# Kernel optimization log

Hardware: AMD Instinct MI355X
Metric: run time of the kernel (lower is better)

## Reference

```python
import jax, jax.numpy as jnp
import numpy as np

B, S, H, I, E, TOP_K = 2, 1024, 1024, 2048, 8, 2


def setup_inputs() -> dict:
    key = jax.random.key(0)
    ks = jax.random.split(key, 5)
    return {
        "hidden_states": jax.random.normal(ks[0], (B, S, H), jnp.float32),
        # torch Linear weights are (out, in)
        "router_w": jax.random.normal(ks[1], (E, H), jnp.float32) * 0.02,
        "w1": jax.random.normal(ks[2], (E, I, H), jnp.float32) * 0.02,
        "v": jax.random.normal(ks[3], (E, I, H), jnp.float32) * 0.02,
        "w2": jax.random.normal(ks[4], (E, H, I), jnp.float32) * 0.02,
    }


def _moe(x, router_w, w1, v, w2):
    # x: [T, H] flattened tokens
    T = x.shape[0]
    n_exp = router_w.shape[0]
    logits = x @ router_w.T                                    # [T, E]
    probs = jax.nn.softmax(logits.astype(jnp.float32), axis=-1)
    top_p, top_i = jax.lax.top_k(probs, TOP_K)                 # [T, K]
    top_p = top_p / top_p.sum(axis=-1, keepdims=True)
    top_p = top_p.astype(x.dtype)
    # dense gate matrix [T, E]; zero for unselected experts -> identical math
    # to the torch gather / index_add combine
    gates = jnp.zeros((T, n_exp), x.dtype).at[
        jnp.arange(T)[:, None], top_i].set(top_p)
    out = jnp.zeros_like(x)
    for e in range(n_exp):  # small fixed expert loop keeps peak memory low
        h = jax.nn.gelu(x @ w1[e].T, approximate=False) * (x @ v[e].T)  # [T, I]
        out = out + gates[:, e:e + 1] * (h @ w2[e].T)                   # [T, H]
    return out, logits


def reference(hidden_states, router_w, w1, v, w2):
    b, s, h = hidden_states.shape
    out, logits = _moe(hidden_states.reshape(-1, h), router_w, w1, v, w2)
    return out.reshape(b, s, h), logits
```

## Files before the change

### kernel.cpp

```cpp
#include <hip/hip_runtime.h>
#include <math.h>

#define T 2048
#define HD 1024
#define ID 2048
#define NE 8
#define CSTRIDE 32

typedef short bf16x8 __attribute__((ext_vector_type(8)));
typedef float f32x4 __attribute__((ext_vector_type(4)));
typedef unsigned short u16x4 __attribute__((ext_vector_type(4)));

__device__ __forceinline__ unsigned short f2bf(float f) {
  union { float f; unsigned u; } v; v.f = f;
  unsigned r = v.u + 0x7FFFu + ((v.u >> 16) & 1u);
  return (unsigned short)(r >> 16);
}

__device__ __forceinline__ void cast_chunk16(const float* __restrict__ s,
                                             unsigned short* __restrict__ d,
                                             size_t base) {
  size_t o = base + (size_t)threadIdx.x * 4;
#pragma unroll
  for (int k = 0; k < 4; k++) {
    float4 f = *(const float4*)(s + o + k * 1024);
    u16x4 h;
    h[0] = f2bf(f.x); h[1] = f2bf(f.y); h[2] = f2bf(f.z); h[3] = f2bf(f.w);
    *(u16x4*)(d + o + k * 1024) = h;
  }
}

__device__ __forceinline__ void glds16(const unsigned short* g, unsigned short* l) {
  __builtin_amdgcn_global_load_lds(
      (const __attribute__((address_space(1))) unsigned int*)(g),
      (__attribute__((address_space(3))) unsigned int*)(l), 16, 0, 0);
}

__global__ __launch_bounds__(256) void prep_kernel(
    const float* __restrict__ x, const float* __restrict__ rw,
    const float* __restrict__ w1, const float* __restrict__ v,
    unsigned short* __restrict__ xb, unsigned short* __restrict__ w1b,
    unsigned short* __restrict__ vb, float* __restrict__ logits_out,
    int* __restrict__ pair_rowid, float* __restrict__ pair_gate,
    int* __restrict__ counts) {
  int bx = blockIdx.x;
  if (bx >= 768) {
    int cid = bx - 768;
    const float* s = (cid < 4096) ? w1 : v;
    unsigned short* d = (cid < 4096) ? w1b : vb;
    cast_chunk16(s, d, (size_t)(cid & 4095) * 4096);
    return;
  }
  if (bx >= 256) {
    cast_chunk16(x, xb, (size_t)(bx - 256) * 4096);
    return;
  }
  __shared__ int s_e[16];
  __shared__ int s_rid[16];
  __shared__ float s_gt[16];
  int tid = threadIdx.x;
  int wid = tid >> 6, lane = tid & 63;
  for (int tk = 0; tk < 2; ++tk) {
    int t = bx * 8 + wid * 2 + tk;
    float acc[NE];
#pragma unroll
    for (int e = 0; e < NE; e++) acc[e] = 0.f;
    const float* xrow = x + (size_t)t * HD;
#pragma unroll 2
    for (int j = 0; j < HD; j += 64) {
      float xv = xrow[j + lane];
#pragma unroll
      for (int e = 0; e < NE; e++) acc[e] += xv * rw[e * HD + j + lane];
    }
#pragma unroll
    for (int e = 0; e < NE; e++)
      for (int off = 32; off > 0; off >>= 1) acc[e] += __shfl_xor(acc[e], off, 64);
    if (lane == 0) {
#pragma unroll
      for (int e = 0; e < NE; e++) logits_out[t * NE + e] = acc[e];
      int e0 = 0;
#pragma unroll
      for (int e = 1; e < NE; e++) if (acc[e] > acc[e0]) e0 = e;
      int e1 = (e0 == 0) ? 1 : 0;
#pragma unroll
      for (int e = 0; e < NE; e++)
        if (e != e0 && e != e1 && acc[e] > acc[e1]) e1 = e;
      float b = __expf(acc[e1] - acc[e0]);
      float g0 = 1.f / (1.f + b);
      float g1 = 1.f - g0;
      int slot = (wid * 2 + tk) * 2;
      s_e[slot] = e0; s_rid[slot] = t * 2;     s_gt[slot] = g0;
      s_e[slot + 1] = e1; s_rid[slot + 1] = t * 2 + 1; s_gt[slot + 1] = g1;
    }
  }
  __syncthreads();
  if (tid < NE) {
    int cnt = 0;
#pragma unroll
    for (int k = 0; k < 16; k++) if (s_e[k] == tid) cnt++;
    if (cnt) {
      int base = atomicAdd(&counts[tid * CSTRIDE], cnt);
      int p = 0;
      for (int k = 0; k < 16; k++)
        if (s_e[k] == tid) {
          pair_rowid[tid * T + base + p] = s_rid[k];
          pair_gate[tid * T + base + p] = s_gt[k];
          p++;
        }
    }
  }
}

__global__ __launch_bounds__(256) void gemm1_kernel(
    const unsigned short* __restrict__ xb, const unsigned short* __restrict__ w1b,
    const unsigned short* __restrict__ vb, unsigned short* __restrict__ hb,
    const float* __restrict__ w2, unsigned short* __restrict__ w2b,
    const int* __restrict__ pair_rowid, const int* __restrict__ counts) {
  if (blockIdx.x >= 32) {
    int cid = (blockIdx.x - 32) + 32 * (blockIdx.y + 16 * blockIdx.z);
    cast_chunk16(w2, w2b, (size_t)cid * 4096);
    return;
  }
  int e = blockIdx.z;
  int cnt = counts[e * CSTRIDE];
  int row0 = blockIdx.y * 128;
  if (row0 >= cnt) return;
  __shared__ unsigned short As[128 * 64];
  __shared__ unsigned short B1s[64 * 64];
  __shared__ unsigned short B2s[64 * 64];
  __shared__ int rids[128];
  int tid = threadIdx.x;
  if (tid < 128) {
    int idx = row0 + tid; if (idx > cnt - 1) idx = cnt - 1;
    rids[tid] = pair_rowid[e * T + idx];
  }
  __syncthreads();
  int lane = tid & 63, wid = tid >> 6;
  int wr = wid >> 1, wc = wid & 1;
  int col0 = blockIdx.x * 64;
  int gr = lane >> 3, gc = lane & 7;
  const unsigned short *aA[4], *aB1[2], *aB2[2];
#pragma unroll
  for (int c = 0; c < 4; c++) {
    int row = (c * 4 + wid) * 8 + gr;
    int tok = rids[row] >> 1;
    aA[c] = xb + (size_t)tok * HD + ((gc ^ (row & 7)) * 8);
  }
#pragma unroll
  for (int c = 0; c < 2; c++) {
    int row = (c * 4 + wid) * 8 + gr;
    int kswz = ((gc ^ (row & 7)) * 8);
    aB1[c] = w1b + ((size_t)(e * ID + col0 + row)) * HD + kswz;
    aB2[c] = vb  + ((size_t)(e * ID + col0 + row)) * HD + kswz;
  }
  f32x4 acc1[4][2] = {};
  f32x4 acc3[4][2] = {};
  int mrow = lane & 15, kq = lane >> 4;
  int swzm = mrow & 7;
  for (int kt = 0; kt < HD; kt += 64) {
#pragma unroll
    for (int c = 0; c < 4; c++)
      glds16(aA[c] + kt, &As[(c * 4 + wid) * 512]);
#pragma unroll
    for (int c = 0; c < 2; c++) {
      glds16(aB1[c] + kt, &B1s[(c * 4 + wid) * 512]);
      glds16(aB2[c] + kt, &B2s[(c * 4 + wid) * 512]);
    }
    __syncthreads();
#pragma unroll
    for (int kk = 0; kk < 2; kk++) {
      int g = kk * 4 + kq;
      int ko = ((g ^ swzm) * 8);
      bf16x8 a[4], b1[2], b2[2];
#pragma unroll
      for (int mi = 0; mi < 4; mi++)
        a[mi] = *(const bf16x8*)&As[(wr * 64 + mi * 16 + mrow) * 64 + ko];
#pragma unroll
      for (int ni = 0; ni < 2; ni++) {
        b1[ni] = *(const bf16x8*)&B1s[(wc * 32 + ni * 16 + mrow) * 64 + ko];
        b2[ni] = *(const bf16x8*)&B2s[(wc * 32 + ni * 16 + mrow) * 64 + ko];
      }
#pragma unroll
      for (int mi = 0; mi < 4; mi++)
#pragma unroll
        for (int ni = 0; ni < 2; ni++) {
          acc1[mi][ni] = __builtin_amdgcn_mfma_f32_16x16x32_bf16(a[mi], b1[ni], acc1[mi][ni], 0, 0, 0);
          acc3[mi][ni] = __builtin_amdgcn_mfma_f32_16x16x32_bf16(a[mi], b2[ni], acc3[mi][ni], 0, 0, 0);
        }
    }
    __syncthreads();
  }
  int dcol = lane & 15, drow4 = (lane >> 4) * 4;
#pragma unroll
  for (int mi = 0; mi < 4; mi++)
#pragma unroll
    for (int ni = 0; ni < 2; ni++)
#pragma unroll
      for (int r = 0; r < 4; r++) {
        int lr = wr * 64 + mi * 16 + drow4 + r;
        if (row0 + lr < cnt) {
          float g1v = acc1[mi][ni][r];
          float g3v = acc3[mi][ni][r];
          float hval = 0.5f * g1v * (1.f + erff(g1v * 0.70710678118654752f)) * g3v;
          int rowid = rids[lr];
          hb[(size_t)rowid * ID + col0 + wc * 32 + ni * 16 + dcol] = f2bf(hval);
        }
      }
}

__global__ __launch_bounds__(256) void gemm2_kernel(
    const unsigned short* __restrict__ hb, const unsigned short* __restrict__ w2b,
    float* __restrict__ yb, const int* __restrict__ pair_rowid,
    const float* __restrict__ pair_gate, const int* __restrict__ counts) {
  int e = blockIdx.z;
  int cnt = counts[e * CSTRIDE];
  int row0 = blockIdx.y * 128;
  if (row0 >= cnt) return;
  __shared__ unsigned short As[128 * 64];
  __shared__ unsigned short Bs[64 * 64];
  __shared__ int rids[128];
  __shared__ float gts[128];
  int tid = threadIdx.x;
  if (tid < 128) {
    int idx = row0 + tid; if (idx > cnt - 1) idx = cnt - 1;
    rids[tid] = pair_rowid[e * T + idx];
    gts[tid] = pair_gate[e * T + idx];
  }
  __syncthreads();
  int lane = tid & 63, wid = tid >> 6;
  int wr = wid >> 1, wc = wid & 1;
  int col0 = blockIdx.x * 64;
  int gr = lane >> 3, gc = lane & 7;
  const unsigned short *aA[4], *aB[2];
#pragma unroll
  for (int c = 0; c < 4; c++) {
    int row = (c * 4 + wid) * 8 + gr;
    aA[c] = hb + (size_t)rids[row] * ID + ((gc ^ (row & 7)) * 8);
  }
#pragma unroll
  for (int c = 0; c < 2; c++) {
    int row = (c * 4 + wid) * 8 + gr;
    int kswz = ((gc ^ (row & 7)) * 8);
    aB[c] = w2b + ((size_t)(e * HD + col0 + row)) * ID + kswz;
  }
  f32x4 acc[4][2] = {};
  int mrow = lane & 15, kq = lane >> 4;
  int swzm = mrow & 7;
  for (int kt = 0; kt < ID; kt += 64) {
#pragma unroll
    for (int c = 0; c < 4; c++)
      glds16(aA[c] + kt, &As[(c * 4 + wid) * 512]);
#pragma unroll
    for (int c = 0; c < 2; c++)
      glds16(aB[c] + kt, &Bs[(c * 4 + wid) * 512]);
    __syncthreads();
#pragma unroll
    for (int kk = 0; kk < 2; kk++) {
      int g = kk * 4 + kq;
      int ko = ((g ^ swzm) * 8);
      bf16x8 a[4], b[2];
#pragma unroll
      for (int mi = 0; mi < 4; mi++)
        a[mi] = *(const bf16x8*)&As[(wr * 64 + mi * 16 + mrow) * 64 + ko];
#pragma unroll
      for (int ni = 0; ni < 2; ni++)
        b[ni] = *(const bf16x8*)&Bs[(wc * 32 + ni * 16 + mrow) * 64 + ko];
#pragma unroll
      for (int mi = 0; mi < 4; mi++)
#pragma unroll
        for (int ni = 0; ni < 2; ni++)
          acc[mi][ni] = __builtin_amdgcn_mfma_f32_16x16x32_bf16(a[mi], b[ni], acc[mi][ni], 0, 0, 0);
    }
    __syncthreads();
  }
  int dcol = lane & 15, drow4 = (lane >> 4) * 4;
#pragma unroll
  for (int mi = 0; mi < 4; mi++)
#pragma unroll
    for (int ni = 0; ni < 2; ni++)
#pragma unroll
      for (int r = 0; r < 4; r++) {
        int lr = wr * 64 + mi * 16 + drow4 + r;
        if (row0 + lr < cnt) {
          float val = gts[lr] * acc[mi][ni][r];
          yb[(size_t)rids[lr] * HD + col0 + wc * 32 + ni * 16 + dcol] = val;
        }
      }
}

__global__ __launch_bounds__(256) void combine_kernel(
    const float* __restrict__ yb, float* __restrict__ out) {
  size_t t = blockIdx.x;
  int c = threadIdx.x * 4;
  float4 a = *(const float4*)(yb + (t * 2) * HD + c);
  float4 b = *(const float4*)(yb + (t * 2 + 1) * HD + c);
  float4 o;
  o.x = a.x + b.x; o.y = a.y + b.y; o.z = a.z + b.z; o.w = a.w + b.w;
  *(float4*)(out + t * HD + c) = o;
}

extern "C" void kernel_launch(void* const* d_in, const int* in_sizes, int n_in,
                              void* d_out, int out_size, void* d_ws, size_t ws_size,
                              hipStream_t stream) {
  const float* x  = (const float*)d_in[0];
  const float* rw = (const float*)d_in[1];
  const float* w1 = (const float*)d_in[2];
  const float* v  = (const float*)d_in[3];
  const float* w2 = (const float*)d_in[4];
  float* out = (float*)d_out;
  float* logits_out = out + (size_t)T * HD;

  char* ws = (char*)d_ws;
  unsigned short* xb  = (unsigned short*)(ws);
  unsigned short* hb  = (unsigned short*)(ws + (4u << 20));
  unsigned short* w1b = (unsigned short*)(ws + (20u << 20));
  unsigned short* vb  = (unsigned short*)(ws + (52u << 20));
  unsigned short* w2b = (unsigned short*)(ws + (84u << 20));
  float* yb           = (float*)(ws + (20u << 20));
  int*   pair_rowid   = (int*)  (ws + (116u << 20));
  float* pair_gate    = (float*)(ws + (116u << 20) + 65536);
  int*   counts       = (int*)  (ws + (116u << 20) + 131072);

  hipMemsetAsync(counts, 0, NE * CSTRIDE * sizeof(int), stream);

  prep_kernel<<<8960, 256, 0, stream>>>(x, rw, w1, v, xb, w1b, vb,
                                        logits_out, pair_rowid, pair_gate,
                                        counts);
  gemm1_kernel<<<dim3(ID / 64 + 32, T / 128, NE), 256, 0, stream>>>(
      xb, w1b, vb, hb, w2, w2b, pair_rowid, counts);
  gemm2_kernel<<<dim3(HD / 64, T / 128, NE), 256, 0, stream>>>(
      hb, w2b, yb, pair_rowid, pair_gate, counts);
  combine_kernel<<<T, 256, 0, stream>>>(yb, out);
}
```

Measured before the change: 320.5 us.

## Split gemm2 over K halves and widen the N tile to 128 columns

The down-projection kernel now computes a 128x128 output tile per block, reusing each loaded A tile across two B tiles, and splits the K=2048 reduction into two halves on separate blocks. Each half writes its partial result to its own yb buffer, and the combine kernel sums four partials instead of two. The aim is to cut redundant reads of the gathered hidden rows and keep enough blocks in flight. The cost is twice the yb write traffic, extra combine reads, and more accumulator registers per thread.

```diff
diff --git a/kernel.cpp b/kernel.cpp
--- a/kernel.cpp
+++ b/kernel.cpp
@@ -212,12 +212,13 @@
     const unsigned short* __restrict__ hb, const unsigned short* __restrict__ w2b,
     float* __restrict__ yb, const int* __restrict__ pair_rowid,
     const float* __restrict__ pair_gate, const int* __restrict__ counts) {
-  int e = blockIdx.z;
+  int e = blockIdx.z >> 1, kh = blockIdx.z & 1;
   int cnt = counts[e * CSTRIDE];
   int row0 = blockIdx.y * 128;
   if (row0 >= cnt) return;
   __shared__ unsigned short As[128 * 64];
-  __shared__ unsigned short Bs[64 * 64];
+  __shared__ unsigned short B1s[64 * 64];
+  __shared__ unsigned short B2s[64 * 64];
   __shared__ int rids[128];
   __shared__ float gts[128];
   int tid = threadIdx.x;
@@ -229,51 +230,60 @@
   __syncthreads();
   int lane = tid & 63, wid = tid >> 6;
   int wr = wid >> 1, wc = wid & 1;
-  int col0 = blockIdx.x * 64;
+  int col0 = blockIdx.x * 128;
   int gr = lane >> 3, gc = lane & 7;
-  const unsigned short *aA[4], *aB[2];
+  const unsigned short *aA[4], *aB1[2], *aB2[2];
 #pragma unroll
   for (int c = 0; c < 4; c++) {
     int row = (c * 4 + wid) * 8 + gr;
-    aA[c] = hb + (size_t)rids[row] * ID + ((gc ^ (row & 7)) * 8);
+    aA[c] = hb + (size_t)rids[row] * ID + kh * 1024 + ((gc ^ (row & 7)) * 8);
   }
 #pragma unroll
   for (int c = 0; c < 2; c++) {
     int row = (c * 4 + wid) * 8 + gr;
     int kswz = ((gc ^ (row & 7)) * 8);
-    aB[c] = w2b + ((size_t)(e * HD + col0 + row)) * ID + kswz;
-  }
-  f32x4 acc[4][2] = {};
+    aB1[c] = w2b + ((size_t)(e * HD + col0 + row)) * ID + kh * 1024 + kswz;
+    aB2[c] = w2b + ((size_t)(e * HD + col0 + 64 + row)) * ID + kh * 1024 + kswz;
+  }
+  f32x4 acc1[4][2] = {};
+  f32x4 acc3[4][2] = {};
   int mrow = lane & 15, kq = lane >> 4;
   int swzm = mrow & 7;
-  for (int kt = 0; kt < ID; kt += 64) {
+  for (int kt = 0; kt < 1024; kt += 64) {
 #pragma unroll
     for (int c = 0; c < 4; c++)
       glds16(aA[c] + kt, &As[(c * 4 + wid) * 512]);
 #pragma unroll
-    for (int c = 0; c < 2; c++)
-      glds16(aB[c] + kt, &Bs[(c * 4 + wid) * 512]);
+    for (int c = 0; c < 2; c++) {
+      glds16(aB1[c] + kt, &B1s[(c * 4 + wid) * 512]);
+      glds16(aB2[c] + kt, &B2s[(c * 4 + wid) * 512]);
+    }
     __syncthreads();
 #pragma unroll
     for (int kk = 0; kk < 2; kk++) {
       int g = kk * 4 + kq;
       int ko = ((g ^ swzm) * 8);
-      bf16x8 a[4], b[2];
+      bf16x8 a[4], b1[2], b2[2];
 #pragma unroll
       for (int mi = 0; mi < 4; mi++)
         a[mi] = *(const bf16x8*)&As[(wr * 64 + mi * 16 + mrow) * 64 + ko];
 #pragma unroll
-      for (int ni = 0; ni < 2; ni++)
-        b[ni] = *(const bf16x8*)&Bs[(wc * 32 + ni * 16 + mrow) * 64 + ko];
+      for (int ni = 0; ni < 2; ni++) {
+        b1[ni] = *(const bf16x8*)&B1s[(wc * 32 + ni * 16 + mrow) * 64 + ko];
+        b2[ni] = *(const bf16x8*)&B2s[(wc * 32 + ni * 16 + mrow) * 64 + ko];
+      }
 #pragma unroll
       for (int mi = 0; mi < 4; mi++)
 #pragma unroll
-        for (int ni = 0; ni < 2; ni++)
-          acc[mi][ni] = __builtin_amdgcn_mfma_f32_16x16x32_bf16(a[mi], b[ni], acc[mi][ni], 0, 0, 0);
+        for (int ni = 0; ni < 2; ni++) {
+          acc1[mi][ni] = __builtin_amdgcn_mfma_f32_16x16x32_bf16(a[mi], b1[ni], acc1[mi][ni], 0, 0, 0);
+          acc3[mi][ni] = __builtin_amdgcn_mfma_f32_16x16x32_bf16(a[mi], b2[ni], acc3[mi][ni], 0, 0, 0);
+        }
     }
     __syncthreads();
   }
   int dcol = lane & 15, drow4 = (lane >> 4) * 4;
+  float* ybh = yb + (size_t)kh * (2 * T) * HD;
 #pragma unroll
   for (int mi = 0; mi < 4; mi++)
 #pragma unroll
@@ -282,8 +292,9 @@
       for (int r = 0; r < 4; r++) {
         int lr = wr * 64 + mi * 16 + drow4 + r;
         if (row0 + lr < cnt) {
-          float val = gts[lr] * acc[mi][ni][r];
-          yb[(size_t)rids[lr] * HD + col0 + wc * 32 + ni * 16 + dcol] = val;
+          size_t rbase = (size_t)rids[lr] * HD + col0 + wc * 32 + ni * 16 + dcol;
+          ybh[rbase] = gts[lr] * acc1[mi][ni][r];
+          ybh[rbase + 64] = gts[lr] * acc3[mi][ni][r];
         }
       }
 }
@@ -292,10 +303,16 @@
     const float* __restrict__ yb, float* __restrict__ out) {
   size_t t = blockIdx.x;
   int c = threadIdx.x * 4;
-  float4 a = *(const float4*)(yb + (t * 2) * HD + c);
-  float4 b = *(const float4*)(yb + (t * 2 + 1) * HD + c);
+  const size_t S = (size_t)(2 * T) * HD;
+  float4 a0 = *(const float4*)(yb + (t * 2) * HD + c);
+  float4 b0 = *(const float4*)(yb + (t * 2 + 1) * HD + c);
+  float4 a1 = *(const float4*)(yb + S + (t * 2) * HD + c);
+  float4 b1 = *(const float4*)(yb + S + (t * 2 + 1) * HD + c);
   float4 o;
-  o.x = a.x + b.x; o.y = a.y + b.y; o.z = a.z + b.z; o.w = a.w + b.w;
+  o.x = a0.x + b0.x + a1.x + b1.x;
+  o.y = a0.y + b0.y + a1.y + b1.y;
+  o.z = a0.z + b0.z + a1.z + b1.z;
+  o.w = a0.w + b0.w + a1.w + b1.w;
   *(float4*)(out + t * HD + c) = o;
 }
 
@@ -328,7 +345,7 @@
                                         counts);
   gemm1_kernel<<<dim3(ID / 64 + 32, T / 128, NE), 256, 0, stream>>>(
       xb, w1b, vb, hb, w2, w2b, pair_rowid, counts);
-  gemm2_kernel<<<dim3(HD / 64, T / 128, NE), 256, 0, stream>>>(
+  gemm2_kernel<<<dim3(HD / 128, T / 128, NE * 2), 256, 0, stream>>>(
       hb, w2b, yb, pair_rowid, pair_gate, counts);
   combine_kernel<<<T, 256, 0, stream>>>(yb, out);
 }
```

New measurement: 323.2 us. About the same (+0.8%).
